# Performance work log

Hardware: AMD Instinct MI355X
Metric: run time of the kernel (lower is better)

Reference implementation:

```python
import jax, jax.numpy as jnp
import numpy as np

ENT_SIZE = 100000; REL_SIZE = 500; ENT_DIM = 256; REL_DIM = 256; H = 256
E = 2048; S = 32; N = 1024; THRESHOLD = 1.0; EPS = 1e-5


def _xav(k, shape):
    fan_in = shape[-1]
    fan_out = shape[-2] if len(shape) > 1 else shape[-1]
    std = (2.0 / (fan_in + fan_out)) ** 0.5
    return jax.random.normal(k, shape, jnp.float32) * std


def setup_inputs() -> dict:
    key = jax.random.key(0)
    ks = jax.random.split(key, 16)
    inp = {}
    inp["neighbors"] = jax.random.randint(ks[0], (E, S), 0, ENT_SIZE)
    inp["pos_h"] = jax.random.randint(ks[1], (N,), 0, E)
    inp["pos_t"] = jax.random.randint(ks[2], (N,), 0, E)
    inp["pos_r"] = jax.random.randint(ks[3], (N,), 0, REL_SIZE)
    inp["neg_h"] = jax.random.randint(ks[4], (N,), 0, E)
    inp["neg_t"] = jax.random.randint(ks[5], (N,), 0, E)
    inp["neg_r"] = jax.random.randint(ks[6], (N,), 0, REL_SIZE)
    inp["ent_embed"] = _xav(ks[7], (ENT_SIZE + 1, ENT_DIM))
    inp["rel_embed"] = _xav(ks[8], (REL_SIZE, REL_DIM))
    inp["trans"] = _xav(ks[9], (2 * REL_SIZE, REL_DIM, ENT_DIM))
    inp["W_ih_f"] = _xav(ks[10], (4 * H, ENT_DIM)); inp["W_hh_f"] = _xav(ks[11], (4 * H, H))
    inp["W_ih_b"] = _xav(ks[12], (4 * H, ENT_DIM)); inp["W_hh_b"] = _xav(ks[13], (4 * H, H))
    inp["b_f"] = jnp.zeros((4 * H,), jnp.float32)
    inp["b_b"] = jnp.zeros((4 * H,), jnp.float32)
    inp["W_lin"] = _xav(ks[14], (ENT_DIM, 2 * H)); inp["b_lin"] = jnp.zeros((ENT_DIM,), jnp.float32)
    inp["gamma"] = jnp.ones((ENT_DIM,), jnp.float32); inp["beta"] = jnp.zeros((ENT_DIM,), jnp.float32)
    return inp


def _lstm_final(x, W_ih, W_hh, b):
    # x: [E,S,D] -> final hidden state [E,H] (PyTorch LSTM gate order i,f,g,o; b = b_ih+b_hh)
    h0 = jnp.zeros((x.shape[0], H), x.dtype)
    def step(carry, xt):
        h, c = carry
        g = xt @ W_ih.T + h @ W_hh.T + b  # [E,4H]
        i, f, gg, o = jnp.split(g, 4, axis=-1)
        c = jax.nn.sigmoid(f) * c + jax.nn.sigmoid(i) * jnp.tanh(gg)
        h = jax.nn.sigmoid(o) * jnp.tanh(c)
        return (h, c), None
    (h, _), _ = jax.lax.scan(step, (h0, h0), jnp.swapaxes(x, 0, 1))
    return h


def _context(ent_embed, neighbors, W_ih_f, W_hh_f, b_f, W_ih_b, W_hh_b, b_b, W_lin, b_lin, gamma, beta):
    x_seq = ent_embed[neighbors]  # [E,S,D]
    h_f = _lstm_final(x_seq, W_ih_f, W_hh_f, b_f)
    h_b = _lstm_final(x_seq[:, ::-1], W_ih_b, W_hh_b, b_b)
    lin = jnp.concatenate([h_f, h_b], -1) @ W_lin.T + b_lin  # [E,ENT_DIM]
    # BatchNorm1d in training mode: batch stats (biased variance)
    mu = lin.mean(0)
    var = lin.var(0)
    return jnp.tanh(gamma * (lin - mu) * jax.lax.rsqrt(var + EPS) + beta)


def _score(trans, rel_embed, ctx, h_idx, r_idx, t_idx):
    Wh = trans[r_idx]             # [N,REL_DIM,ENT_DIM] (grouped expert GEMV, batched)
    Wt = trans[r_idx + REL_SIZE]
    d = jnp.einsum('nre,ne->nr', Wh, ctx[h_idx]) - jnp.einsum('nre,ne->nr', Wt, ctx[t_idx])
    return jnp.linalg.norm(d + rel_embed[r_idx], axis=1)


def reference(neighbors, pos_h, pos_t, pos_r, neg_h, neg_t, neg_r,
              ent_embed, rel_embed, trans, W_ih_f, W_hh_f, W_ih_b, W_hh_b,
              b_f, b_b, W_lin, b_lin, gamma, beta):
    ctx = _context(ent_embed, neighbors, W_ih_f, W_hh_f, b_f, W_ih_b, W_hh_b, b_b,
                   W_lin, b_lin, gamma, beta)
    pos_n = _score(trans, rel_embed, ctx, pos_h, pos_r, pos_t)
    neg_n = _score(trans, rel_embed, ctx, neg_h, neg_r, neg_t)
    return jnp.sum(pos_n + jax.nn.relu(THRESHOLD - neg_n))
```

## Files before the change

### kernel.cpp

```cpp
#include <hip/hip_runtime.h>

constexpr int kE   = 2048;
constexpr int kS   = 32;
constexpr int kD   = 256;
constexpr int kK   = 512;
constexpr int kREL = 500;
constexpr int kN   = 1024;

typedef unsigned short u16;
typedef __attribute__((ext_vector_type(8))) _Float16 f16x8;
typedef __attribute__((ext_vector_type(4))) float    f32x4;
typedef __attribute__((ext_vector_type(4))) unsigned short us4;

static __device__ __forceinline__ u16 f2h(float f) {
  _Float16 h = (_Float16)f;
  return __builtin_bit_cast(u16, h);
}
static __device__ __forceinline__ float h2f(u16 v) {
  _Float16 h = __builtin_bit_cast(_Float16, v);
  return (float)h;
}
static __device__ __forceinline__ float sigf(float x) { return 1.f / (1.f + __expf(-x)); }
static __device__ __forceinline__ float tanhfast(float x) {
  float e = __expf(2.f * x);
  return 1.f - 2.f / (e + 1.f);
}
static __device__ __forceinline__ void gl_lds16(const void* g, void* l) {
  __builtin_amdgcn_global_load_lds((const __attribute__((address_space(1))) unsigned int*)g,
                                   (__attribute__((address_space(3))) unsigned int*)l, 16, 0, 0);
}

__global__ void prep_gather(const float* __restrict__ Wih_f, const float* __restrict__ Whh_f,
                            const float* __restrict__ Wih_b, const float* __restrict__ Whh_b,
                            const float* __restrict__ Wlin_in,
                            const int* __restrict__ neighbors, const float* __restrict__ ent,
                            u16* __restrict__ Wv3, u16* __restrict__ Whhr,
                            u16* __restrict__ Wlin, u16* __restrict__ ximg) {
  if (blockIdx.x < 576) {
    int idx = blockIdx.x * 256 + threadIdx.x;
    if (idx < 65536) {
      int q  = idx & 2047;
      int ch = (idx >> 11) & 3;
      int y  = (idx >> 13) & 3;
      int d  = idx >> 15;
      int j  = q >> 3;
      int k8 = (q & 7) ^ (j & 7);
      int jg = y * 256 + j;
      int g = (jg >> 4) & 3, u = (jg >> 6) * 16 + (jg & 15);
      int R = g * 256 + u;
      int k = ch * 64 + k8 * 8;
      const float* src = (d ? Wih_b : Wih_f) + R * 256 + k;
      ushort oa[8];
#pragma unroll
      for (int i = 0; i < 8; i++) oa[i] = f2h(src[i]);
      *(uint4*)((char*)Wv3 + (size_t)idx * 16) = *(uint4*)oa;
    } else if (idx < 131072) {
      int i2 = idx - 65536;
      int d = i2 >> 15;
      int j = (i2 & 32767) >> 5;
      int k = (i2 & 31) * 8;
      int g = (j >> 4) & 3, u = (j >> 6) * 16 + (j & 15);
      int R = g * 256 + u;
      const float* src = (d ? Whh_b : Whh_f) + R * 256 + k;
      ushort oa[8];
#pragma unroll
      for (int i = 0; i < 8; i++) oa[i] = f2h(src[i]);
      *(uint4*)((char*)Whhr + (size_t)i2 * 16) = *(uint4*)oa;
    } else if (idx < 131072 + 16384) {
      int q = (idx - 131072) * 8;
#pragma unroll
      for (int i = 0; i < 8; i++) Wlin[q + i] = f2h(Wlin_in[q + i]);
    }
  } else {
    int idx = (blockIdx.x - 576) * 256 + threadIdx.x;
    int q    = idx & 511;
    int ch   = (idx >> 9) & 3;
    int tile = (idx >> 11) & 31;
    int s    = idx >> 16;
    int row = q >> 3;
    int c8 = (q & 7) ^ (row & 7);
    int e = tile * 64 + row;
    int k = ch * 64 + c8 * 8;
    int nb = neighbors[e * 32 + s];
    const float* src = ent + (size_t)nb * 256 + k;
    float4 v0 = *(const float4*)src;
    float4 v1 = *(const float4*)(src + 4);
    ushort oa[8];
    oa[0] = f2h(v0.x); oa[1] = f2h(v0.y); oa[2] = f2h(v0.z); oa[3] = f2h(v0.w);
    oa[4] = f2h(v1.x); oa[5] = f2h(v1.y); oa[6] = f2h(v1.z); oa[7] = f2h(v1.w);
    *(uint4*)((char*)ximg + (size_t)idx * 16) = *(uint4*)oa;
  }
}

__global__ __launch_bounds__(256) void xgemm(
    const u16* __restrict__ ximg, const u16* __restrict__ Wv3,
    const float* __restrict__ b_f, const float* __restrict__ b_b,
    u16* __restrict__ gx) {
  __shared__ __align__(16) char As[8192];
  __shared__ __align__(16) char Bs[32768];
  const int tid = threadIdx.x, lane = tid & 63, w = tid >> 6;
  const int l15 = lane & 15, lq = lane >> 4;
  const int ts = blockIdx.x >> 5;
  const int etile = blockIdx.x & 31;
  const int y = blockIdx.y, dir = blockIdx.z;
  const int e0 = etile * 64;
  const int s = dir ? (31 - ts) : ts;
  const char* imgA = (const char*)ximg + (size_t)(s * 32 + etile) * 32768;
  const char* imgB = (const char*)Wv3 + (size_t)(dir * 4 + y) * 131072;
  const float* bd = dir ? b_b : b_f;
  const int u = (y * 4 + w) * 16 + l15;

  f32x4 acc[4][4];
#pragma unroll
  for (int n = 0; n < 4; n++) {
    float bv = bd[n * 256 + u];
#pragma unroll
    for (int m = 0; m < 4; m++) acc[m][n] = (f32x4){bv, bv, bv, bv};
  }

  for (int ch = 0; ch < 4; ++ch) {
#pragma unroll
    for (int i = 0; i < 2; i++)
      gl_lds16(imgA + ch * 8192 + i * 4096 + w * 1024 + lane * 16,
               As + i * 4096 + w * 1024);
#pragma unroll
    for (int i = 0; i < 8; i++)
      gl_lds16(imgB + (size_t)ch * 32768 + i * 4096 + w * 1024 + lane * 16,
               Bs + i * 4096 + w * 1024);
    __syncthreads();
#pragma unroll
    for (int ks = 0; ks < 2; ++ks) {
      const int kb = ks * 64 + lq * 16;
      f16x8 a[4], b[4];
#pragma unroll
      for (int m = 0; m < 4; m++) {
        int row = m * 16 + l15;
        a[m] = *(const f16x8*)(As + row * 128 + (kb ^ ((row & 7) << 4)));
      }
#pragma unroll
      for (int n = 0; n < 4; n++) {
        int row = w * 64 + n * 16 + l15;
        b[n] = *(const f16x8*)(Bs + row * 128 + (kb ^ ((row & 7) << 4)));
      }
#pragma unroll
      for (int m = 0; m < 4; m++)
#pragma unroll
        for (int n = 0; n < 4; n++)
          acc[m][n] = __builtin_amdgcn_mfma_f32_16x16x32_f16(a[m], b[n], acc[m][n], 0, 0, 0);
    }
    __syncthreads();
  }

  u16* out = gx + ((size_t)(dir * kS + ts) * kE) * 1024;
#pragma unroll
  for (int m = 0; m < 4; m++)
#pragma unroll
    for (int r = 0; r < 4; r++) {
      int e = e0 + m * 16 + lq * 4 + r;
      us4 o;
      o[0] = f2h(acc[m][0][r]); o[1] = f2h(acc[m][1][r]);
      o[2] = f2h(acc[m][2][r]); o[3] = f2h(acc[m][3][r]);
      __builtin_nontemporal_store(o, (us4*)(out + ((size_t)e * 256 + u) * 4));
    }
}

__global__ __launch_bounds__(256) void lstm_step(
    const u16* __restrict__ gx, const u16* __restrict__ Whhr,
    const u16* __restrict__ hprev, u16* __restrict__ hnext,
    float* __restrict__ cbuf, int t) {
  const int tid = threadIdx.x, lane = tid & 63, w = tid >> 6;
  const int l15 = lane & 15, lq = lane >> 4;
  const int bid = blockIdx.x;
  const int dir = bid >> 8;
  const int rem = bid & 255;
  const int jg = rem >> 6;
  const int et = rem & 63;
  const int e0 = et * 32;
  const int c0 = jg * 256 + w * 64;
  const int unit = (c0 >> 6) * 16 + l15;

  const u16* Wd  = Whhr + ((size_t)dir * 1024 + c0) * kD;
  const u16* hpd = hprev + (size_t)dir * kE * kD;
  u16* hnd = hnext + (size_t)dir * kE * kD;
  float* cd = cbuf + (size_t)dir * kE * kD;
  const u16* gp = gx + ((size_t)(dir * kS + t) * kE) * 1024;

  f32x4 acc[2][4];
#pragma unroll
  for (int m = 0; m < 2; m++)
#pragma unroll
    for (int r = 0; r < 4; r++) {
      us4 g = __builtin_nontemporal_load(
          (const us4*)(gp + (size_t)(e0 + m * 16 + lq * 4 + r) * 1024 + unit * 4));
#pragma unroll
      for (int n = 0; n < 4; n++) acc[m][n][r] = h2f(g[n]);
    }

  const int klane = lq * 8;
#pragma unroll
  for (int ks = 0; ks < 8; ks++) {
    const int ka = ks * 32 + klane;
    f16x8 a[2], b[4];
#pragma unroll
    for (int m = 0; m < 2; m++)
      a[m] = *(const f16x8*)(hpd + (size_t)(e0 + m * 16 + l15) * kD + ka);
#pragma unroll
    for (int n = 0; n < 4; n++)
      b[n] = *(const f16x8*)(Wd + (size_t)(n * 16 + l15) * kD + ka);
#pragma unroll
    for (int m = 0; m < 2; m++)
#pragma unroll
      for (int n = 0; n < 4; n++)
        acc[m][n] = __builtin_amdgcn_mfma_f32_16x16x32_f16(a[m], b[n], acc[m][n], 0, 0, 0);
  }

#pragma unroll
  for (int m = 0; m < 2; m++)
#pragma unroll
    for (int r = 0; r < 4; r++) {
      int row = e0 + m * 16 + lq * 4 + r;
      size_t off = (size_t)row * kD + unit;
      float gi = acc[m][0][r];
      float gf = acc[m][1][r];
      float gg = acc[m][2][r];
      float go = acc[m][3][r];
      float c_old = cd[off];
      float cn = sigf(gf) * c_old + sigf(gi) * tanhfast(gg);
      cd[off] = cn;
      hnd[off] = f2h(sigf(go) * tanhfast(cn));
    }
}

static __device__ __forceinline__ void gemm_tile(
    const u16* __restrict__ Alo, const u16* __restrict__ Ahi,
    const u16* __restrict__ W, int e0,
    u16* As, u16* Bs, f32x4 (&acc)[4][4]) {
  const int tid = threadIdx.x;
  const int lane = tid & 63;
  const int w = tid >> 6;
#pragma unroll
  for (int m = 0; m < 4; m++)
#pragma unroll
    for (int n = 0; n < 4; n++) acc[m][n] = (f32x4){0.f, 0.f, 0.f, 0.f};

  for (int ch = 0; ch < 8; ++ch) {
    const int k0 = ch * 64;
    __syncthreads();
    const u16* Asrc = (k0 < 256) ? Alo : Ahi;
    const int kbase = (k0 < 256) ? k0 : (k0 - 256);
#pragma unroll
    for (int i = 0; i < 2; i++) {
      int idx = tid + i * 256;
      int row = idx >> 3, c8 = idx & 7;
      uint4 v = *(const uint4*)(Asrc + (size_t)(e0 + row) * 256 + kbase + c8 * 8);
      *(uint4*)((char*)As + row * 128 + ((c8 * 16) ^ ((row & 7) << 4))) = v;
    }
#pragma unroll
    for (int i = 0; i < 8; i++) {
      int idx = tid + i * 256;
      int j = idx >> 3, c8 = idx & 7;
      uint4 v = *(const uint4*)(W + (size_t)j * kK + k0 + c8 * 8);
      *(uint4*)((char*)Bs + j * 128 + ((c8 * 16) ^ ((j & 7) << 4))) = v;
    }
    __syncthreads();
#pragma unroll
    for (int ks = 0; ks < 2; ++ks) {
      const int kb = ks * 64 + (lane >> 4) * 16;
      f16x8 a[4], b[4];
#pragma unroll
      for (int m = 0; m < 4; m++) {
        int row = m * 16 + (lane & 15);
        a[m] = *(const f16x8*)((const char*)As + row * 128 + (kb ^ ((row & 7) << 4)));
      }
#pragma unroll
      for (int n = 0; n < 4; n++) {
        int row = w * 64 + n * 16 + (lane & 15);
        b[n] = *(const f16x8*)((const char*)Bs + row * 128 + (kb ^ ((row & 7) << 4)));
      }
#pragma unroll
      for (int m = 0; m < 4; m++)
#pragma unroll
        for (int n = 0; n < 4; n++)
          acc[m][n] = __builtin_amdgcn_mfma_f32_16x16x32_f16(a[m], b[n], acc[m][n], 0, 0, 0);
    }
  }
}

__global__ __launch_bounds__(256) void lin_kernel(
    const u16* __restrict__ hf, const u16* __restrict__ hb,
    const u16* __restrict__ Wl, const float* __restrict__ b_lin,
    float* __restrict__ lin, float* __restrict__ part) {
  __shared__ __align__(16) char smem[40960];
  u16* As = (u16*)smem;
  u16* Bs = (u16*)(smem + 8192);
  const int tid = threadIdx.x, lane = tid & 63, w = tid >> 6;
  const int l15 = lane & 15, lq = lane >> 4;
  const int e0 = blockIdx.x * 64;
  f32x4 acc[4][4];
  gemm_tile(hf, hb, Wl, e0, As, Bs, acc);
#pragma unroll
  for (int n = 0; n < 4; n++) {
    int col = w * 64 + n * 16 + l15;
    float bl = b_lin[col];
    float s1 = 0.f, s2 = 0.f;
#pragma unroll
    for (int m = 0; m < 4; m++)
#pragma unroll
      for (int r = 0; r < 4; r++) {
        int e = e0 + m * 16 + lq * 4 + r;
        float v = acc[m][n][r] + bl;
        lin[(size_t)e * 256 + col] = v;
        s1 += v; s2 += v * v;
      }
    s1 += __shfl_down(s1, 16); s2 += __shfl_down(s2, 16);
    s1 += __shfl_down(s1, 32); s2 += __shfl_down(s2, 32);
    if (lq == 0) {
      part[blockIdx.x * 256 + col] = s1;
      part[8192 + blockIdx.x * 256 + col] = s2;
    }
  }
}

__global__ void bn_apply(const float* __restrict__ lin, const float* __restrict__ part,
                         const float* __restrict__ gamma, const float* __restrict__ beta,
                         float* __restrict__ ctx) {
  int c = threadIdx.x;
  float s = 0.f, s2 = 0.f;
  for (int b = 0; b < 32; b++) { s += part[b * 256 + c]; s2 += part[8192 + b * 256 + c]; }
  float mu = s * (1.f / 2048.f);
  float rsig = rsqrtf(s2 * (1.f / 2048.f) - mu * mu + 1e-5f);
  float ga = gamma[c], be = beta[c];
  int e0 = blockIdx.x * 8;
  for (int e = e0; e < e0 + 8; ++e) {
    float x = lin[(size_t)e * 256 + c];
    ctx[(size_t)e * 256 + c] = tanhf(ga * (x - mu) * rsig + be);
  }
}

__global__ void group_rel(const int* __restrict__ pr, const int* __restrict__ nr,
                          int* __restrict__ offs, int* __restrict__ list) {
  __shared__ int cnt[512], sc[512], cur[512];
  int tid = threadIdx.x;
  cnt[tid] = 0;
  __syncthreads();
  for (int i = tid; i < 2 * kN; i += 512) {
    int r = (i < kN) ? pr[i] : nr[i - kN];
    atomicAdd(&cnt[r], 1);
  }
  __syncthreads();
  sc[tid] = cnt[tid];
  __syncthreads();
  for (int d = 1; d < 512; d <<= 1) {
    int v = (tid >= d) ? sc[tid - d] : 0;
    __syncthreads();
    sc[tid] += v;
    __syncthreads();
  }
  int excl = (tid == 0) ? 0 : sc[tid - 1];
  cur[tid] = excl;
  if (tid <= kREL) offs[tid] = excl;
  __syncthreads();
  for (int i = tid; i < 2 * kN; i += 512) {
    int r = (i < kN) ? pr[i] : nr[i - kN];
    int p = atomicAdd(&cur[r], 1);
    list[p] = i;
  }
}

template <int NJ>
static __device__ __forceinline__ void score_body(
    const float* __restrict__ ctx, const float* __restrict__ trans,
    const float* __restrict__ rel_embed,
    const int* __restrict__ ph, const int* __restrict__ pt,
    const int* __restrict__ nh, const int* __restrict__ nt,
    const int* __restrict__ list, float* __restrict__ sqacc,
    int r, int half, int start, int G,
    float* csh, float* cst, float (*red)[4], int* tidx) {
  const int tid = threadIdx.x;
#pragma unroll
  for (int j = 0; j < NJ; j++) {
    float vh = 0.f, vt = 0.f;
    if (j < G) {
      int i = list[start + j];
      int hh = (i < kN) ? ph[i] : nh[i - kN];
      int tt = (i < kN) ? pt[i] : nt[i - kN];
      vh = ctx[(size_t)hh * 256 + tid];
      vt = ctx[(size_t)tt * 256 + tid];
      if (tid == 0) tidx[j] = i;
    }
    csh[j * 256 + tid] = vh;
    cst[j * 256 + tid] = vt;
  }
  __syncthreads();

  const int row = half * 128 + (tid >> 1);
  const int q4b = (tid & 1) * 32;
  const float4* whp = (const float4*)(trans + (size_t)r * 65536 + (size_t)row * 256) + q4b;
  const float4* wtp = (const float4*)(trans + ((size_t)r + kREL) * 65536 + (size_t)row * 256) + q4b;
  const float4* ch4 = (const float4*)csh;
  const float4* ct4 = (const float4*)cst;

  float acc[NJ];
#pragma unroll
  for (int j = 0; j < NJ; j++) acc[j] = 0.f;

  for (int line = 0; line < 4; line++) {
    float4 wh[8], wt[8];
#pragma unroll
    for (int i = 0; i < 8; i++) { wh[i] = whp[line * 8 + i]; wt[i] = wtp[line * 8 + i]; }
#pragma unroll
    for (int q4 = 0; q4 < 8; q4++) {
      const int qa = q4b + line * 8 + q4;
#pragma unroll
      for (int j = 0; j < NJ; j++) {
        float4 xh = ch4[j * 64 + qa];
        float4 xt = ct4[j * 64 + qa];
        acc[j] += wh[q4].x * xh.x + wh[q4].y * xh.y + wh[q4].z * xh.z + wh[q4].w * xh.w
                - (wt[q4].x * xt.x + wt[q4].y * xt.y + wt[q4].z * xt.z + wt[q4].w * xt.w);
      }
    }
  }

  const float rv = rel_embed[r * 256 + row];
#pragma unroll
  for (int j = 0; j < NJ; j++) {
    float d = acc[j] + __shfl_xor(acc[j], 1) + rv;
    float v = d * d;
    v += __shfl_down(v, 32); v += __shfl_down(v, 16);
    v += __shfl_down(v, 8);  v += __shfl_down(v, 4);
    v += __shfl_down(v, 2);  v += __shfl_down(v, 1);
    if ((tid & 63) == 0) red[j][tid >> 6] = v;
  }
  __syncthreads();
  if (tid < G) {
    float s = (red[tid][0] + red[tid][1] + red[tid][2] + red[tid][3]) * 0.5f;
    atomicAdd(&sqacc[tidx[tid]], s);
  }
  __syncthreads();
}

__global__ __launch_bounds__(256) void score_grouped(
    const float* __restrict__ ctx, const float* __restrict__ trans,
    const float* __restrict__ rel_embed,
    const int* __restrict__ ph, const int* __restrict__ pt,
    const int* __restrict__ nh, const int* __restrict__ nt,
    const int* __restrict__ offs, const int* __restrict__ list,
    float* __restrict__ sqacc) {
  const int r = blockIdx.x >> 1, half = blockIdx.x & 1;
  int start = offs[r], end = offs[r + 1];
  if (start >= end) return;
  __shared__ float csh[16 * 256];
  __shared__ float cst[16 * 256];
  __shared__ float red[16][4];
  __shared__ int tidx[16];
  for (int c = start; c < end; c += 16) {
    int G = min(16, end - c);
    if (G <= 4)
      score_body<4>(ctx, trans, rel_embed, ph, pt, nh, nt, list, sqacc, r, half, c, G,
                    csh, cst, red, tidx);
    else if (G <= 8)
      score_body<8>(ctx, trans, rel_embed, ph, pt, nh, nt, list, sqacc, r, half, c, G,
                    csh, cst, red, tidx);
    else
      score_body<16>(ctx, trans, rel_embed, ph, pt, nh, nt, list, sqacc, r, half, c, G,
                     csh, cst, red, tidx);
  }
}

__global__ void final_reduce(const float* __restrict__ sqacc, float* __restrict__ out) {
  int tid = threadIdx.x;
  float a = 0.f;
  for (int i = tid; i < 2 * kN; i += 256) {
    float s = sqrtf(sqacc[i]);
    a += (i < kN) ? s : fmaxf(0.f, 1.f - s);
  }
  for (int off = 32; off; off >>= 1) a += __shfl_down(a, off);
  __shared__ float w4[4];
  if ((tid & 63) == 0) w4[tid >> 6] = a;
  __syncthreads();
  if (tid == 0) out[0] = w4[0] + w4[1] + w4[2] + w4[3];
}

extern "C" void kernel_launch(void* const* d_in, const int* in_sizes, int n_in,
                              void* d_out, int out_size, void* d_ws, size_t ws_size,
                              hipStream_t stream) {
  const int*   neighbors = (const int*)d_in[0];
  const int*   pos_h = (const int*)d_in[1];
  const int*   pos_t = (const int*)d_in[2];
  const int*   pos_r = (const int*)d_in[3];
  const int*   neg_h = (const int*)d_in[4];
  const int*   neg_t = (const int*)d_in[5];
  const int*   neg_r = (const int*)d_in[6];
  const float* ent_embed = (const float*)d_in[7];
  const float* rel_embed = (const float*)d_in[8];
  const float* trans = (const float*)d_in[9];
  const float* W_ih_f = (const float*)d_in[10];
  const float* W_hh_f = (const float*)d_in[11];
  const float* W_ih_b = (const float*)d_in[12];
  const float* W_hh_b = (const float*)d_in[13];
  const float* b_f = (const float*)d_in[14];
  const float* b_b = (const float*)d_in[15];
  const float* W_lin = (const float*)d_in[16];
  const float* b_lin = (const float*)d_in[17];
  const float* gamma = (const float*)d_in[18];
  const float* beta = (const float*)d_in[19];

  char* ws = (char*)d_ws;
  size_t off = 0;
  auto alloc = [&](size_t bytes) {
    void* p = ws + off;
    off = (off + bytes + 255) & ~(size_t)255;
    return p;
  };
  u16* Wv3    = (u16*)alloc((size_t)65536 * 16);
  u16* Whhr   = (u16*)alloc((size_t)2 * 1024 * kD * 2);
  u16* Wlin   = (u16*)alloc((size_t)256 * kK * 2);
  u16* ximg   = (u16*)alloc((size_t)2097152 * 16);
  u16* h0     = (u16*)alloc((size_t)2 * kE * kD * 2);
  u16* h1     = (u16*)alloc((size_t)2 * kE * kD * 2);
  float* cbuf = (float*)alloc((size_t)2 * kE * kD * 4);
  u16* gx     = (u16*)alloc((size_t)2 * kS * kE * 1024 * 2);
  float* lin  = (float*)alloc((size_t)kE * 256 * 4);
  float* part = (float*)alloc((size_t)2 * 32 * 256 * 4);
  float* ctx  = (float*)alloc((size_t)kE * 256 * 4);
  float* sqacc = (float*)alloc((size_t)2 * kN * 4);
  int* offsb  = (int*)alloc((size_t)512 * 4);
  int* list   = (int*)alloc((size_t)2 * kN * 4);
  (void)in_sizes; (void)n_in; (void)out_size; (void)ws_size;

  hipMemsetAsync(h0, 0, (size_t)2 * kE * kD * 2, stream);
  hipMemsetAsync(cbuf, 0, (size_t)2 * kE * kD * 4, stream);
  hipMemsetAsync(sqacc, 0, (size_t)2 * kN * 4, stream);

  prep_gather<<<576 + 8192, 256, 0, stream>>>(W_ih_f, W_hh_f, W_ih_b, W_hh_b, W_lin,
                                              neighbors, ent_embed,
                                              Wv3, Whhr, Wlin, ximg);
  group_rel<<<1, 512, 0, stream>>>(pos_r, neg_r, offsb, list);

  xgemm<<<dim3(1024, 4, 2), 256, 0, stream>>>(ximg, Wv3, b_f, b_b, gx);

  for (int t = 0; t < kS; t++) {
    const u16* hp = (t & 1) ? h1 : h0;
    u16* hn = (t & 1) ? h0 : h1;
    lstm_step<<<512, 256, 0, stream>>>(gx, Whhr, hp, hn, cbuf, t);
  }

  lin_kernel<<<32, 256, 0, stream>>>(h0, h0 + (size_t)kE * kD, Wlin, b_lin, lin, part);
  bn_apply<<<256, 256, 0, stream>>>(lin, part, gamma, beta, ctx);
  score_grouped<<<2 * kREL, 256, 0, stream>>>(ctx, trans, rel_embed,
                                              pos_h, pos_t, neg_h, neg_t, offsb, list, sqacc);
  final_reduce<<<1, 256, 0, stream>>>(sqacc, (float*)d_out);
}
```

Before: 804.9 us.

## Double-buffer xgemm K-chunks and split LSTM step and scoring across more blocks

The input-projection GEMM now stages 32-wide K chunks into double-buffered LDS, so the next chunk is prefetched while the current one is multiplied. The weight and gathered-activation images are re-laid out to match, with a new XOR swizzle. Separately, each lstm_step block now covers 16 entities instead of 32 and the launch doubles to 1024 blocks. score_grouped splits each relation over four row quarters instead of two. The aim is better latency hiding and more parallelism across CUs, at the cost of reloading the recurrent weights more often and running more atomics and blocks.

Measured after the change: 1.362 ms. +69.3%, slower.

```diff
diff --git a/kernel.cpp b/kernel.cpp
--- a/kernel.cpp
+++ b/kernel.cpp
@@ -34,26 +34,27 @@
                             const float* __restrict__ Wih_b, const float* __restrict__ Whh_b,
                             const float* __restrict__ Wlin_in,
                             const int* __restrict__ neighbors, const float* __restrict__ ent,
-                            u16* __restrict__ Wv3, u16* __restrict__ Whhr,
+                            u16* __restrict__ Wv4, u16* __restrict__ Whhr,
                             u16* __restrict__ Wlin, u16* __restrict__ ximg) {
   if (blockIdx.x < 576) {
     int idx = blockIdx.x * 256 + threadIdx.x;
     if (idx < 65536) {
-      int q  = idx & 2047;
-      int ch = (idx >> 11) & 3;
+      int q  = idx & 1023;
+      int ch = (idx >> 10) & 7;
       int y  = (idx >> 13) & 3;
       int d  = idx >> 15;
-      int j  = q >> 3;
-      int k8 = (q & 7) ^ (j & 7);
+      int j   = q >> 2;
+      int sub = q & 3;
+      int ks  = sub ^ ((j >> 1) & 3);
       int jg = y * 256 + j;
       int g = (jg >> 4) & 3, u = (jg >> 6) * 16 + (jg & 15);
       int R = g * 256 + u;
-      int k = ch * 64 + k8 * 8;
+      int k = ch * 32 + ks * 8;
       const float* src = (d ? Wih_b : Wih_f) + R * 256 + k;
       ushort oa[8];
 #pragma unroll
       for (int i = 0; i < 8; i++) oa[i] = f2h(src[i]);
-      *(uint4*)((char*)Wv3 + (size_t)idx * 16) = *(uint4*)oa;
+      *(uint4*)((char*)Wv4 + (size_t)idx * 16) = *(uint4*)oa;
     } else if (idx < 131072) {
       int i2 = idx - 65536;
       int d = i2 >> 15;
@@ -73,14 +74,16 @@
     }
   } else {
     int idx = (blockIdx.x - 576) * 256 + threadIdx.x;
-    int q    = idx & 511;
-    int ch   = (idx >> 9) & 3;
-    int tile = (idx >> 11) & 31;
-    int s    = idx >> 16;
-    int row = q >> 3;
-    int c8 = (q & 7) ^ (row & 7);
+    int q    = idx & 255;
+    int ch   = (idx >> 8) & 7;
+    int img  = idx >> 11;
+    int tile = img & 31;
+    int s    = img >> 5;
+    int row = q >> 2;
+    int sub = q & 3;
+    int ks  = sub ^ ((row >> 1) & 3);
     int e = tile * 64 + row;
-    int k = ch * 64 + c8 * 8;
+    int k = ch * 32 + ks * 8;
     int nb = neighbors[e * 32 + s];
     const float* src = ent + (size_t)nb * 256 + k;
     float4 v0 = *(const float4*)src;
@@ -93,11 +96,11 @@
 }
 
 __global__ __launch_bounds__(256) void xgemm(
-    const u16* __restrict__ ximg, const u16* __restrict__ Wv3,
+    const u16* __restrict__ ximg, const u16* __restrict__ Wv4,
     const float* __restrict__ b_f, const float* __restrict__ b_b,
     u16* __restrict__ gx) {
-  __shared__ __align__(16) char As[8192];
-  __shared__ __align__(16) char Bs[32768];
+  __shared__ __align__(16) char As[2][4096];
+  __shared__ __align__(16) char Bs[2][16384];
   const int tid = threadIdx.x, lane = tid & 63, w = tid >> 6;
   const int l15 = lane & 15, lq = lane >> 4;
   const int ts = blockIdx.x >> 5;
@@ -106,7 +109,7 @@
   const int e0 = etile * 64;
   const int s = dir ? (31 - ts) : ts;
   const char* imgA = (const char*)ximg + (size_t)(s * 32 + etile) * 32768;
-  const char* imgB = (const char*)Wv3 + (size_t)(dir * 4 + y) * 131072;
+  const char* imgB = (const char*)Wv4 + (size_t)(dir * 4 + y) * 131072;
   const float* bd = dir ? b_b : b_f;
   const int u = (y * 4 + w) * 16 + l15;
 
@@ -118,37 +121,36 @@
     for (int m = 0; m < 4; m++) acc[m][n] = (f32x4){bv, bv, bv, bv};
   }
 
-  for (int ch = 0; ch < 4; ++ch) {
-#pragma unroll
-    for (int i = 0; i < 2; i++)
-      gl_lds16(imgA + ch * 8192 + i * 4096 + w * 1024 + lane * 16,
-               As + i * 4096 + w * 1024);
-#pragma unroll
-    for (int i = 0; i < 8; i++)
-      gl_lds16(imgB + (size_t)ch * 32768 + i * 4096 + w * 1024 + lane * 16,
-               Bs + i * 4096 + w * 1024);
+  auto stage = [&](int c, int buf) {
+    gl_lds16(imgA + (size_t)c * 4096 + w * 1024 + lane * 16, As[buf] + w * 1024);
+#pragma unroll
+    for (int i = 0; i < 4; i++)
+      gl_lds16(imgB + (size_t)c * 16384 + (w * 4 + i) * 1024 + lane * 16,
+               Bs[buf] + (w * 4 + i) * 1024);
+  };
+
+  stage(0, 0);
+  for (int c = 0; c < 8; ++c) {
     __syncthreads();
-#pragma unroll
-    for (int ks = 0; ks < 2; ++ks) {
-      const int kb = ks * 64 + lq * 16;
-      f16x8 a[4], b[4];
-#pragma unroll
-      for (int m = 0; m < 4; m++) {
-        int row = m * 16 + l15;
-        a[m] = *(const f16x8*)(As + row * 128 + (kb ^ ((row & 7) << 4)));
-      }
-#pragma unroll
-      for (int n = 0; n < 4; n++) {
-        int row = w * 64 + n * 16 + l15;
-        b[n] = *(const f16x8*)(Bs + row * 128 + (kb ^ ((row & 7) << 4)));
-      }
-#pragma unroll
-      for (int m = 0; m < 4; m++)
-#pragma unroll
-        for (int n = 0; n < 4; n++)
-          acc[m][n] = __builtin_amdgcn_mfma_f32_16x16x32_f16(a[m], b[n], acc[m][n], 0, 0, 0);
-    }
-    __syncthreads();
+    if (c + 1 < 8) stage(c + 1, (c + 1) & 1);
+    const char* Ab = As[c & 1];
+    const char* Bb = Bs[c & 1];
+    f16x8 a[4], b[4];
+#pragma unroll
+    for (int m = 0; m < 4; m++) {
+      int row = m * 16 + l15;
+      a[m] = *(const f16x8*)(Ab + row * 64 + ((lq ^ ((row >> 1) & 3)) << 4));
+    }
+#pragma unroll
+    for (int n = 0; n < 4; n++) {
+      int row = w * 64 + n * 16 + l15;
+      b[n] = *(const f16x8*)(Bb + row * 64 + ((lq ^ ((row >> 1) & 3)) << 4));
+    }
+#pragma unroll
+    for (int m = 0; m < 4; m++)
+#pragma unroll
+      for (int n = 0; n < 4; n++)
+        acc[m][n] = __builtin_amdgcn_mfma_f32_16x16x32_f16(a[m], b[n], acc[m][n], 0, 0, 0);
   }
 
   u16* out = gx + ((size_t)(dir * kS + ts) * kE) * 1024;
@@ -171,11 +173,11 @@
   const int tid = threadIdx.x, lane = tid & 63, w = tid >> 6;
   const int l15 = lane & 15, lq = lane >> 4;
   const int bid = blockIdx.x;
-  const int dir = bid >> 8;
-  const int rem = bid & 255;
-  const int jg = rem >> 6;
-  const int et = rem & 63;
-  const int e0 = et * 32;
+  const int dir = bid >> 9;
+  const int rem = bid & 511;
+  const int jg = rem >> 7;
+  const int et = rem & 127;
+  const int e0 = et * 16;
   const int c0 = jg * 256 + w * 64;
   const int unit = (c0 >> 6) * 16 + l15;
 
@@ -185,50 +187,42 @@
   float* cd = cbuf + (size_t)dir * kE * kD;
   const u16* gp = gx + ((size_t)(dir * kS + t) * kE) * 1024;
 
-  f32x4 acc[2][4];
-#pragma unroll
-  for (int m = 0; m < 2; m++)
-#pragma unroll
-    for (int r = 0; r < 4; r++) {
-      us4 g = __builtin_nontemporal_load(
-          (const us4*)(gp + (size_t)(e0 + m * 16 + lq * 4 + r) * 1024 + unit * 4));
-#pragma unroll
-      for (int n = 0; n < 4; n++) acc[m][n][r] = h2f(g[n]);
-    }
+  f32x4 acc[4];
+#pragma unroll
+  for (int r = 0; r < 4; r++) {
+    us4 g = __builtin_nontemporal_load(
+        (const us4*)(gp + (size_t)(e0 + lq * 4 + r) * 1024 + unit * 4));
+#pragma unroll
+    for (int n = 0; n < 4; n++) acc[n][r] = h2f(g[n]);
+  }
 
   const int klane = lq * 8;
 #pragma unroll
   for (int ks = 0; ks < 8; ks++) {
     const int ka = ks * 32 + klane;
-    f16x8 a[2], b[4];
-#pragma unroll
-    for (int m = 0; m < 2; m++)
-      a[m] = *(const f16x8*)(hpd + (size_t)(e0 + m * 16 + l15) * kD + ka);
+    f16x8 a0, b[4];
+    a0 = *(const f16x8*)(hpd + (size_t)(e0 + l15) * kD + ka);
 #pragma unroll
     for (int n = 0; n < 4; n++)
       b[n] = *(const f16x8*)(Wd + (size_t)(n * 16 + l15) * kD + ka);
 #pragma unroll
-    for (int m = 0; m < 2; m++)
-#pragma unroll
-      for (int n = 0; n < 4; n++)
-        acc[m][n] = __builtin_amdgcn_mfma_f32_16x16x32_f16(a[m], b[n], acc[m][n], 0, 0, 0);
-  }
-
-#pragma unroll
-  for (int m = 0; m < 2; m++)
-#pragma unroll
-    for (int r = 0; r < 4; r++) {
-      int row = e0 + m * 16 + lq * 4 + r;
-      size_t off = (size_t)row * kD + unit;
-      float gi = acc[m][0][r];
-      float gf = acc[m][1][r];
-      float gg = acc[m][2][r];
-      float go = acc[m][3][r];
-      float c_old = cd[off];
-      float cn = sigf(gf) * c_old + sigf(gi) * tanhfast(gg);
-      cd[off] = cn;
-      hnd[off] = f2h(sigf(go) * tanhfast(cn));
-    }
+    for (int n = 0; n < 4; n++)
+      acc[n] = __builtin_amdgcn_mfma_f32_16x16x32_f16(a0, b[n], acc[n], 0, 0, 0);
+  }
+
+#pragma unroll
+  for (int r = 0; r < 4; r++) {
+    int row = e0 + lq * 4 + r;
+    size_t off = (size_t)row * kD + unit;
+    float gi = acc[0][r];
+    float gf = acc[1][r];
+    float gg = acc[2][r];
+    float go = acc[3][r];
+    float c_old = cd[off];
+    float cn = sigf(gf) * c_old + sigf(gi) * tanhfast(gg);
+    cd[off] = cn;
+    hnd[off] = f2h(sigf(go) * tanhfast(cn));
+  }
 }
 
 static __device__ __forceinline__ void gemm_tile(
@@ -374,7 +368,7 @@
     const int* __restrict__ ph, const int* __restrict__ pt,
     const int* __restrict__ nh, const int* __restrict__ nt,
     const int* __restrict__ list, float* __restrict__ sqacc,
-    int r, int half, int start, int G,
+    int r, int quarter, int start, int G,
     float* csh, float* cst, float (*red)[4], int* tidx) {
   const int tid = threadIdx.x;
 #pragma unroll
@@ -393,8 +387,8 @@
   }
   __syncthreads();
 
-  const int row = half * 128 + (tid >> 1);
-  const int q4b = (tid & 1) * 32;
+  const int row = quarter * 64 + (tid >> 2);
+  const int q4b = (tid & 3) * 16;
   const float4* whp = (const float4*)(trans + (size_t)r * 65536 + (size_t)row * 256) + q4b;
   const float4* wtp = (const float4*)(trans + ((size_t)r + kREL) * 65536 + (size_t)row * 256) + q4b;
   const float4* ch4 = (const float4*)csh;
@@ -404,7 +398,7 @@
 #pragma unroll
   for (int j = 0; j < NJ; j++) acc[j] = 0.f;
 
-  for (int line = 0; line < 4; line++) {
+  for (int line = 0; line < 2; line++) {
     float4 wh[8], wt[8];
 #pragma unroll
     for (int i = 0; i < 8; i++) { wh[i] = whp[line * 8 + i]; wt[i] = wtp[line * 8 + i]; }
@@ -424,8 +418,9 @@
   const float rv = rel_embed[r * 256 + row];
 #pragma unroll
   for (int j = 0; j < NJ; j++) {
-    float d = acc[j] + __shfl_xor(acc[j], 1) + rv;
-    float v = d * d;
+    float d1 = acc[j] + __shfl_xor(acc[j], 1);
+    float d = d1 + __shfl_xor(d1, 2) + rv;
+    float v = d * d * 0.25f;
     v += __shfl_down(v, 32); v += __shfl_down(v, 16);
     v += __shfl_down(v, 8);  v += __shfl_down(v, 4);
     v += __shfl_down(v, 2);  v += __shfl_down(v, 1);
@@ -433,7 +428,7 @@
   }
   __syncthreads();
   if (tid < G) {
-    float s = (red[tid][0] + red[tid][1] + red[tid][2] + red[tid][3]) * 0.5f;
+    float s = red[tid][0] + red[tid][1] + red[tid][2] + red[tid][3];
     atomicAdd(&sqacc[tidx[tid]], s);
   }
   __syncthreads();
@@ -446,7 +441,7 @@
     const int* __restrict__ nh, const int* __restrict__ nt,
     const int* __restrict__ offs, const int* __restrict__ list,
     float* __restrict__ sqacc) {
-  const int r = blockIdx.x >> 1, half = blockIdx.x & 1;
+  const int r = blockIdx.x >> 2, quarter = blockIdx.x & 3;
   int start = offs[r], end = offs[r + 1];
   if (start >= end) return;
   __shared__ float csh[16 * 256];
@@ -456,13 +451,13 @@
   for (int c = start; c < end; c += 16) {
     int G = min(16, end - c);
     if (G <= 4)
-      score_body<4>(ctx, trans, rel_embed, ph, pt, nh, nt, list, sqacc, r, half, c, G,
+      score_body<4>(ctx, trans, rel_embed, ph, pt, nh, nt, list, sqacc, r, quarter, c, G,
                     csh, cst, red, tidx);
     else if (G <= 8)
-      score_body<8>(ctx, trans, rel_embed, ph, pt, nh, nt, list, sqacc, r, half, c, G,
+      score_body<8>(ctx, trans, rel_embed, ph, pt, nh, nt, list, sqacc, r, quarter, c, G,
                     csh, cst, red, tidx);
     else
-      score_body<16>(ctx, trans, rel_embed, ph, pt, nh, nt, list, sqacc, r, half, c, G,
+      score_body<16>(ctx, trans, rel_embed, ph, pt, nh, nt, list, sqacc, r, quarter, c, G,
                      csh, cst, red, tidx);
   }
 }
@@ -512,7 +507,7 @@
     off = (off + bytes + 255) & ~(size_t)255;
     return p;
   };
-  u16* Wv3    = (u16*)alloc((size_t)65536 * 16);
+  u16* Wv4    = (u16*)alloc((size_t)65536 * 16);
   u16* Whhr   = (u16*)alloc((size_t)2 * 1024 * kD * 2);
   u16* Wlin   = (u16*)alloc((size_t)256 * kK * 2);
   u16* ximg   = (u16*)alloc((size_t)2097152 * 16);
@@ -534,20 +529,20 @@
 
   prep_gather<<<576 + 8192, 256, 0, stream>>>(W_ih_f, W_hh_f, W_ih_b, W_hh_b, W_lin,
                                               neighbors, ent_embed,
-                                              Wv3, Whhr, Wlin, ximg);
+                                              Wv4, Whhr, Wlin, ximg);
   group_rel<<<1, 512, 0, stream>>>(pos_r, neg_r, offsb, list);
 
-  xgemm<<<dim3(1024, 4, 2), 256, 0, stream>>>(ximg, Wv3, b_f, b_b, gx);
+  xgemm<<<dim3(1024, 4, 2), 256, 0, stream>>>(ximg, Wv4, b_f, b_b, gx);
 
   for (int t = 0; t < kS; t++) {
     const u16* hp = (t & 1) ? h1 : h0;
     u16* hn = (t & 1) ? h0 : h1;
-    lstm_step<<<512, 256, 0, stream>>>(gx, Whhr, hp, hn, cbuf, t);
+    lstm_step<<<1024, 256, 0, stream>>>(gx, Whhr, hp, hn, cbuf, t);
   }
 
   lin_kernel<<<32, 256, 0, stream>>>(h0, h0 + (size_t)kE * kD, Wlin, b_lin, lin, part);
   bn_apply<<<256, 256, 0, stream>>>(lin, part, gamma, beta, ctx);
-  score_grouped<<<2 * kREL, 256, 0, stream>>>(ctx, trans, rel_embed,
+  score_grouped<<<4 * kREL, 256, 0, stream>>>(ctx, trans, rel_embed,
                                               pos_h, pos_t, neg_h, neg_t, offsb, list, sqacc);
   final_reduce<<<1, 256, 0, stream>>>(sqacc, (float*)d_out);
 }
```
